# Kernel optimization log

Hardware: AMD Instinct MI355X
Metric: run time of the kernel (lower is better)

Reference implementation:

```python
import jax, jax.numpy as jnp
import numpy as np

# ---- static config (mirrors init_kwargs) ----
H, N, HKV = 32, 64, 8
HN = H * N            # model dim 2048
KV_DIM = HKV * N      # 512
B, T = 2, 1024
EPS = 1e-6
ROPE_THETA = 1.0e6
SPLITS_WAVGK = (96, 96, 64, 256, 64)   # xw, xa, xv, xg, xk lora ranks
SPLITS_RKV = (HN, KV_DIM, KV_DIM)


def rms_norm(x, w, eps=EPS):
    xf = x.astype(jnp.float32)
    var = jnp.mean(xf * xf, axis=-1, keepdims=True)
    return (w * (xf * jax.lax.rsqrt(var + eps))).astype(x.dtype)


def rotate_half(x):
    x1, x2 = jnp.split(x, 2, axis=-1)
    return jnp.concatenate((-x2, x1), axis=-1)


def apply_rope(q, k, cos, sin):
    # q:[B,T,H,N], k:[B,T,HKV,N], cos/sin:[B,T,N] -> unsqueeze head dim (unsqueeze_dim=2)
    cos = cos[:, :, None, :]
    sin = sin[:, :, None, :]
    return q * cos + rotate_half(q) * sin, k * cos + rotate_half(k) * sin


def rwkv7_recurrence(r, gk, k, v, a, b, S0):
    # fused_recurrent_rwkv7 (head_first=False). All inputs [B,T,H,N] fp32, S0 [B,H,N_key,N_val].
    # S_t = diag(exp(gk_t)) S_{t-1} + b_t (a_t^T S_{t-1}) + k_t v_t^T ;  o_t = r_t^T S_t
    def step(S, inp):
        r_t, w_t, k_t, v_t, a_t, b_t = inp
        sa = jnp.einsum('bhk,bhkv->bhv', a_t, S)
        S = (jnp.exp(w_t)[..., None] * S
             + k_t[..., None] * v_t[..., None, :]
             + b_t[..., None] * sa[..., None, :])
        o = jnp.einsum('bhk,bhkv->bhv', r_t, S)
        return S, o
    xs = tuple(jnp.swapaxes(t, 0, 1) for t in (r, gk, k, v, a, b))  # [T,B,H,N]
    S, o = jax.lax.scan(step, S0, xs)
    return jnp.swapaxes(o, 0, 1), S


def setup_inputs() -> dict:
    key = jax.random.key(0)
    ks = jax.random.split(key, 24)
    f32 = jnp.float32
    rn = lambda k, shape, s=1.0: jax.random.normal(k, shape, dtype=f32) * s

    x_in = rn(ks[0], (B, T, HN))
    v_first = rn(ks[1], (B, T, HKV, N))
    k_first = rn(ks[2], (B, T, HKV, N))
    state = jnp.zeros((B, H, N, N), f32)

    # real rope cache (faithful to get_batch_rope_cache output) at positions 0..T-1
    inv_freq = 1.0 / (ROPE_THETA ** (np.arange(0, N, 2, dtype=np.float32) / N))
    freqs = np.outer(np.arange(T, dtype=np.float32), inv_freq)  # [T, N/2]
    emb = np.concatenate([freqs, freqs], axis=-1)               # [T, N]
    calc_cos = jnp.broadcast_to(jnp.asarray(np.cos(emb), dtype=np.float32), (B, T, N))
    calc_sin = jnp.broadcast_to(jnp.asarray(np.sin(emb), dtype=np.float32), (B, T, N))

    wavgk1 = rn(ks[3], (HN, sum(SPLITS_WAVGK)), 0.02)
    w0 = rn(ks[4], (HN,), 0.5)
    w2 = rn(ks[5], (SPLITS_WAVGK[0], HN), 0.02)
    a0 = rn(ks[6], (HN,), 0.1)
    a2 = rn(ks[7], (SPLITS_WAVGK[1], HN), 0.02)
    v0 = rn(ks[8], (KV_DIM,), 0.1)
    v2 = rn(ks[9], (SPLITS_WAVGK[2], KV_DIM), 0.02)
    g2 = rn(ks[10], (SPLITS_WAVGK[3], HN), 0.02)
    k0 = rn(ks[11], (KV_DIM,), 0.1)
    k2 = rn(ks[12], (SPLITS_WAVGK[4], KV_DIM), 0.02)
    r_k = rn(ks[13], (H, N), 0.1)
    RKV = rn(ks[14], (HN, HN + 2 * KV_DIM), 0.02)   # fpx weight, dequantized form
    O = rn(ks[15], (HN, HN), 0.02)
    R_bias = rn(ks[16], (HN,), 0.02)
    K_bias = rn(ks[17], (KV_DIM,), 0.02)
    V_bias = rn(ks[18], (KV_DIM,), 0.02)
    ln_r = jnp.ones((N,), f32)
    ln_k = jnp.ones((N,), f32)
    ln1 = jnp.ones((HN,), f32)
    ln2 = jnp.ones((HN,), f32)

    return dict(x_in=x_in, v_first=v_first, k_first=k_first, state=state,
                calc_cos=calc_cos, calc_sin=calc_sin, wavgk1=wavgk1,
                w0=w0, w2=w2, a0=a0, a2=a2, v0=v0, v2=v2, g2=g2, k0=k0, k2=k2,
                r_k=r_k, RKV=RKV, O=O, R_bias=R_bias, K_bias=K_bias, V_bias=V_bias,
                ln_r=ln_r, ln_k=ln_k, ln1=ln1, ln2=ln2)


def reference(x_in, v_first, k_first, state, calc_cos, calc_sin, wavgk1,
              w0, w2, a0, a2, v0, v2, g2, k0, k2, r_k, RKV, O,
              R_bias, K_bias, V_bias, ln_r, ln_k, ln1, ln2):
    Bx, Tx, C = x_in.shape
    kv_repeat = HN // KV_DIM  # GQA repeat factor (4)

    x = rms_norm(x_in, ln1)
    xw, xa, xv, xg, xk = jnp.split(x @ wavgk1, np.cumsum(SPLITS_WAVGK)[:-1].tolist(), axis=-1)

    rkv = x @ RKV  # fpx_matmul -> dense matmul on dequantized weight
    r, k, v = jnp.split(rkv, np.cumsum(SPLITS_RKV)[:-1].tolist(), axis=-1)
    r = (r + R_bias).reshape(Bx, Tx, H, N)
    k = (k + K_bias).reshape(Bx, Tx, HKV, N)
    v = (v + V_bias).reshape(Bx, Tx, HKV, N)

    r = rms_norm(r, ln_r)
    k = rms_norm(k, ln_k)
    r, k = apply_rope(r, k, calc_cos, calc_sin)

    # layer_id = 1 (> 0): mix with first-layer value/key
    v = v + (v_first - v) * jax.nn.sigmoid(xv @ v2 + v0).reshape(Bx, Tx, HKV, N)
    k = k + (k_first - k) * jax.nn.sigmoid(xk @ k2 + k0).reshape(Bx, Tx, HKV, N)

    # repeat_kv: [B,T,HKV,N] -> [B,T,H,N] -> [B,T,HN]
    k = jnp.repeat(k, kv_repeat, axis=2).reshape(Bx, Tx, HN)
    v = jnp.repeat(v, kv_repeat, axis=2).reshape(Bx, Tx, HN)

    a = jax.nn.sigmoid(xa @ a2 + a0)  # in-context learning rate gate [B,T,HN]
    k4 = k.reshape(Bx, Tx, H, N)
    kk = (k4 / jnp.maximum(jnp.linalg.norm(k4, axis=-1, keepdims=True), 1e-12)).reshape(Bx, Tx, HN)

    w_log = -jax.nn.softplus(-(jnp.tanh(xw) @ w2 + w0)) - 0.5  # log-decay, <= -0.5
    k = k * (1.0 - w_log + a)
    aa = -kk
    bb = kk * a
    gk = -jnp.exp(w_log.astype(jnp.float32))  # passed to fused_recurrent_rwkv7 as log decay

    shp = (Bx, Tx, H, N)
    o, state_out = rwkv7_recurrence(
        r.reshape(shp).astype(jnp.float32), gk.reshape(shp),
        k.reshape(shp).astype(jnp.float32), v.reshape(shp).astype(jnp.float32),
        aa.reshape(shp).astype(jnp.float32), bb.reshape(shp).astype(jnp.float32),
        state.astype(jnp.float32))

    xx = o.reshape(Bx, Tx, HN) * (float(N) ** -0.5)
    bonus = ((r * k.reshape(shp) * r_k).sum(axis=-1, keepdims=True) * v.reshape(shp)).reshape(Bx, Tx, HN)
    xx = xx.astype(x_in.dtype) + bonus

    out = (xx * (jax.nn.sigmoid(xg) @ g2)) @ O  # fpx output projection
    x_new = x_in + out
    return rms_norm(x_new, ln2)
```

## Files before the change

### kernel.cpp

```cpp
#include <hip/hip_runtime.h>

typedef unsigned short u16;
typedef unsigned int u32;

using f32x4 = __attribute__((ext_vector_type(4))) float;
using bf16x8 = __attribute__((ext_vector_type(8))) __bf16;

#define HN 2048
#define KVD 512
#define TOKENS 2048
#define N1 3712
#define K2W 576
#define N2 7168

#define OFF_Y1   0ull
#define OFF_OO   0ull
#define OFF_XG   16777216ull
#define OFF_Y2   30408704ull
#define OFF_OUTR 30408704ull
#define OFF_BT1  89128960ull
#define OFF_XB   104333312ull
#define OFF_W2T  89128960ull
#define OFF_X2   97386496ull
#define OFF_OT   89128960ull
#define OFF_RR   112721920ull
#define OFF_DEC  129499136ull
#define OFF_KR   146276352ull
#define OFF_VV   163053568ull
#define OFF_AA   179830784ull
#define OFF_BB   196608000ull
#define WS_NEED  213385216ull

__device__ __forceinline__ u16 f2bf(float f) {
    u32 u = __float_as_uint(f);
    u32 r = u + 0x7fffu + ((u >> 16) & 1u);
    return (u16)(r >> 16);
}
__device__ __forceinline__ float sigm(float x) { return 1.f / (1.f + expf(-x)); }
__device__ __forceinline__ float wsum(float v) {
#pragma unroll
    for (int m = 32; m > 0; m >>= 1) v += __shfl_xor(v, m, 64);
    return v;
}
__device__ __forceinline__ float rowsum16(float v) {
    float t;
    t = __uint_as_float(__builtin_amdgcn_update_dpp(0, __float_as_uint(v), 0x121, 0xf, 0xf, true));
    v += t;
    t = __uint_as_float(__builtin_amdgcn_update_dpp(0, __float_as_uint(v), 0x122, 0xf, 0xf, true));
    v += t;
    t = __uint_as_float(__builtin_amdgcn_update_dpp(0, __float_as_uint(v), 0x124, 0xf, 0xf, true));
    v += t;
    t = __uint_as_float(__builtin_amdgcn_update_dpp(0, __float_as_uint(v), 0x128, 0xf, 0xf, true));
    v += t;
    return v;
}

typedef __attribute__((address_space(1))) const void glob_t;
typedef __attribute__((address_space(3))) void lds_t;
__device__ __forceinline__ void gload_lds16(const void* g, void* l) {
    __builtin_amdgcn_global_load_lds((glob_t*)g, (lds_t*)l, 16, 0, 0);
}

template<int OFF>
__device__ __forceinline__ float4 ds_read128(u32 a) {
    float4 r;
    asm volatile("ds_read_b128 %0, %1 offset:%2" : "=v"(r) : "v"(a), "i"(OFF));
    return r;
}
template<int OFF>
__device__ __forceinline__ float ds_read32(u32 a) {
    float r;
    asm volatile("ds_read_b32 %0, %1 offset:%2" : "=v"(r) : "v"(a), "i"(OFF));
    return r;
}

__global__ __launch_bounds__(256) void k_prep_bt1(const float* __restrict__ wavgk1,
                                                  const float* __restrict__ RKV,
                                                  u16* __restrict__ BT1) {
    __shared__ float tile[64][65];
    const int bn = blockIdx.x >> 5;
    const int bk = blockIdx.x & 31;
    const int n0 = bn << 6, k0 = bk << 6;
    const int c = threadIdx.x & 63, q = threadIdx.x >> 6;
#pragma unroll
    for (int i = 0; i < 16; ++i) {
        const int r = (q << 4) + i;
        float v = 0.f;
        if (bn < 9)       v = wavgk1[(size_t)(k0 + r) * 576 + n0 + c];
        else if (bn < 57) v = RKV[(size_t)(k0 + r) * 3072 + (n0 + c - 576)];
        tile[r][c] = v;
    }
    __syncthreads();
#pragma unroll
    for (int i = 0; i < 16; ++i) {
        const int rw = (q << 4) + i;
        BT1[(size_t)(n0 + rw) * 2048 + k0 + c] = f2bf(tile[c][rw]);
    }
}

__global__ __launch_bounds__(256) void k_prep_w2t(const float* __restrict__ w2, const float* __restrict__ a2,
                                                  const float* __restrict__ g2, const float* __restrict__ v2,
                                                  const float* __restrict__ k2, u16* __restrict__ W2T) {
    int idx = blockIdx.x * 256 + threadIdx.x;
    int n = idx / 576, c = idx - n * 576;
    float v = 0.f;
    if (n < 2048)      { if (c < 96)              v = w2[(size_t)c * 2048 + n]; }
    else if (n < 4096) { if (c >= 96 && c < 192)  v = a2[(size_t)(c - 96) * 2048 + (n - 2048)]; }
    else if (n < 6144) { if (c >= 192 && c < 448) v = g2[(size_t)(c - 192) * 2048 + (n - 4096)]; }
    else if (n < 6656) { if (c >= 448 && c < 512) v = v2[(size_t)(c - 448) * 512 + (n - 6144)]; }
    else               { if (c >= 512)            v = k2[(size_t)(c - 512) * 512 + (n - 6656)]; }
    W2T[idx] = f2bf(v);
}

__global__ __launch_bounds__(256) void k_prep_ot(const float* __restrict__ O, u16* __restrict__ OT) {
    __shared__ float tile[64][65];
    const int bn = blockIdx.x >> 5, bk = blockIdx.x & 31;
    const int n0 = bn << 6, k0 = bk << 6;
    const int c = threadIdx.x & 63, q = threadIdx.x >> 6;
#pragma unroll
    for (int i = 0; i < 16; ++i) {
        const int r = (q << 4) + i;
        tile[r][c] = O[(size_t)(k0 + r) * 2048 + n0 + c];
    }
    __syncthreads();
#pragma unroll
    for (int i = 0; i < 16; ++i) {
        const int rw = (q << 4) + i;
        OT[(size_t)(n0 + rw) * 2048 + k0 + c] = f2bf(tile[c][rw]);
    }
}

__global__ __launch_bounds__(256) void k_rms1(const float* __restrict__ X,
                                              const float* __restrict__ ln1,
                                              u16* __restrict__ XB) {
    const int t = blockIdx.x, tid = threadIdx.x;
    const float* row = X + ((size_t)t << 11);
    float4 v0 = *(const float4*)(row + tid * 8);
    float4 v1 = *(const float4*)(row + tid * 8 + 4);
    float ss = v0.x*v0.x + v0.y*v0.y + v0.z*v0.z + v0.w*v0.w
             + v1.x*v1.x + v1.y*v1.y + v1.z*v1.z + v1.w*v1.w;
    ss = wsum(ss);
    __shared__ float red[4];
    if ((tid & 63) == 0) red[tid >> 6] = ss;
    __syncthreads();
    float scale = rsqrtf((red[0] + red[1] + red[2] + red[3]) * (1.f / 2048.f) + 1e-6f);
    float4 w0_ = *(const float4*)(ln1 + tid * 8);
    float4 w1_ = *(const float4*)(ln1 + tid * 8 + 4);
    u16* o = XB + ((size_t)t << 11) + tid * 8;
    o[0] = f2bf(v0.x * scale * w0_.x); o[1] = f2bf(v0.y * scale * w0_.y);
    o[2] = f2bf(v0.z * scale * w0_.z); o[3] = f2bf(v0.w * scale * w0_.w);
    o[4] = f2bf(v1.x * scale * w1_.x); o[5] = f2bf(v1.y * scale * w1_.y);
    o[6] = f2bf(v1.z * scale * w1_.z); o[7] = f2bf(v1.w * scale * w1_.w);
}

__global__ __launch_bounds__(256) void k_gemm(const u16* __restrict__ A,
                                              const u16* __restrict__ Bt,
                                              float* __restrict__ C,
                                              int M, int N, int K) {
    __shared__ __align__(16) u16 tA[4096];
    __shared__ __align__(16) u16 tB[4096];
    const int tid = threadIdx.x;
    const int w = tid >> 6, l = tid & 63;
    const int bm = blockIdx.x << 7, bn = blockIdx.y << 7;
    const int wm = (w >> 1) << 6, wn = (w & 1) << 6;
    const int lrow = l >> 2;
    const int lk = (((l & 3) ^ ((l >> 3) & 3)) << 3);
    f32x4 acc[4][4] = {};
    const size_t rA0 = (size_t)(bm + (w << 4) + lrow) * K;
    const size_t rA1 = (size_t)(bm + ((w + 4) << 4) + lrow) * K;
    const size_t rB0 = (size_t)(bn + (w << 4) + lrow) * K;
    const size_t rB1 = (size_t)(bn + ((w + 4) << 4) + lrow) * K;
    const int frow = l & 15;
    const int koff = (((l >> 4) ^ ((l >> 1) & 3)) << 3);
    for (int kt = 0; kt < K; kt += 32) {
        gload_lds16(A + rA0 + kt + lk, &tA[w << 9]);
        gload_lds16(A + rA1 + kt + lk, &tA[2048 + (w << 9)]);
        gload_lds16(Bt + rB0 + kt + lk, &tB[w << 9]);
        gload_lds16(Bt + rB1 + kt + lk, &tB[2048 + (w << 9)]);
        __syncthreads();
        bf16x8 av[4], bv[4];
#pragma unroll
        for (int i = 0; i < 4; ++i) {
            av[i] = *(const bf16x8*)&tA[((wm + (i << 4) + frow) << 5) + koff];
            bv[i] = *(const bf16x8*)&tB[((wn + (i << 4) + frow) << 5) + koff];
        }
#pragma unroll
        for (int i = 0; i < 4; ++i)
#pragma unroll
            for (int j = 0; j < 4; ++j)
                acc[i][j] = __builtin_amdgcn_mfma_f32_16x16x32_bf16(av[i], bv[j], acc[i][j], 0, 0, 0);
        __syncthreads();
    }
    const int crow = bm + wm + ((l >> 4) << 2);
    const int ccol = bn + wn + (l & 15);
#pragma unroll
    for (int i = 0; i < 4; ++i)
#pragma unroll
        for (int j = 0; j < 4; ++j)
#pragma unroll
            for (int jj = 0; jj < 4; ++jj)
                C[(size_t)(crow + (i << 4) + jj) * N + ccol + (j << 4)] = acc[i][j][jj];
}

__global__ __launch_bounds__(256) void k_gemm2(const u16* __restrict__ A,
                                               const u16* __restrict__ Bt,
                                               float* __restrict__ C) {
    __shared__ __align__(16) u16 tA[4096];
    __shared__ __align__(16) u16 tB[4096];
    const int tid = threadIdx.x;
    const int w = tid >> 6, l = tid & 63;
    const int by = blockIdx.y;
    int c0, K;
    if (by < 16)      { c0 = 0;   K = 96; }
    else if (by < 32) { c0 = 96;  K = 96; }
    else if (by < 48) { c0 = 192; K = 256; }
    else if (by < 52) { c0 = 448; K = 64; }
    else              { c0 = 512; K = 64; }
    const int n0 = by << 7;
    const int bm = blockIdx.x << 7;
    const int wm = (w >> 1) << 6, wn = (w & 1) << 6;
    const int lrow = l >> 2;
    const int lk = (((l & 3) ^ ((l >> 3) & 3)) << 3);
    f32x4 acc[4][4] = {};
    const size_t rA0 = (size_t)(bm + (w << 4) + lrow) * 576 + c0;
    const size_t rA1 = (size_t)(bm + ((w + 4) << 4) + lrow) * 576 + c0;
    const size_t rB0 = (size_t)(n0 + (w << 4) + lrow) * 576 + c0;
    const size_t rB1 = (size_t)(n0 + ((w + 4) << 4) + lrow) * 576 + c0;
    const int frow = l & 15;
    const int koff = (((l >> 4) ^ ((l >> 1) & 3)) << 3);
    for (int kt = 0; kt < K; kt += 32) {
        gload_lds16(A + rA0 + kt + lk, &tA[w << 9]);
        gload_lds16(A + rA1 + kt + lk, &tA[2048 + (w << 9)]);
        gload_lds16(Bt + rB0 + kt + lk, &tB[w << 9]);
        gload_lds16(Bt + rB1 + kt + lk, &tB[2048 + (w << 9)]);
        __syncthreads();
        bf16x8 av[4], bv[4];
#pragma unroll
        for (int i = 0; i < 4; ++i) {
            av[i] = *(const bf16x8*)&tA[((wm + (i << 4) + frow) << 5) + koff];
            bv[i] = *(const bf16x8*)&tB[((wn + (i << 4) + frow) << 5) + koff];
        }
#pragma unroll
        for (int i = 0; i < 4; ++i)
#pragma unroll
            for (int j = 0; j < 4; ++j)
                acc[i][j] = __builtin_amdgcn_mfma_f32_16x16x32_bf16(av[i], bv[j], acc[i][j], 0, 0, 0);
        __syncthreads();
    }
    const int crow = bm + wm + ((l >> 4) << 2);
    const int ccol = n0 + wn + (l & 15);
#pragma unroll
    for (int i = 0; i < 4; ++i)
#pragma unroll
        for (int j = 0; j < 4; ++j)
#pragma unroll
            for (int jj = 0; jj < 4; ++jj)
                C[(size_t)(crow + (i << 4) + jj) * N2 + ccol + (j << 4)] = acc[i][j][jj];
}

__global__ __launch_bounds__(256) void k_prep_x2(const float* __restrict__ Y1, u16* __restrict__ X2) {
    int idx = blockIdx.x * 256 + threadIdx.x;
    int t = idx / 576, c = idx - t * 576;
    const float* y1 = Y1 + (size_t)t * N1;
    float v;
    if (c < 96)       v = tanhf(y1[c]);
    else if (c < 192) v = y1[c];
    else if (c < 448) v = sigm(y1[c + 64]);
    else if (c < 512) v = y1[c - 256];
    else              v = y1[c];
    X2[idx] = f2bf(v);
}

__global__ __launch_bounds__(256) void k_prep_rec(
    const float* __restrict__ Y1, const float* __restrict__ Y2,
    const float* __restrict__ v_first, const float* __restrict__ k_first,
    const float* __restrict__ cosb, const float* __restrict__ sinb,
    const float* __restrict__ w0, const float* __restrict__ a0,
    const float* __restrict__ v0b, const float* __restrict__ k0b,
    const float* __restrict__ R_bias, const float* __restrict__ K_bias,
    const float* __restrict__ V_bias, const float* __restrict__ ln_r,
    const float* __restrict__ ln_k,
    float* __restrict__ RR, float* __restrict__ DEC, float* __restrict__ KR,
    float* __restrict__ VV, float* __restrict__ AA, float* __restrict__ BB) {
    const int t = blockIdx.x, tid = threadIdx.x;
    const int ww = tid >> 6, lane = tid & 63;
    const float* y1 = Y1 + (size_t)t * N1;
    const float* y2 = Y2 + (size_t)t * N2;
    const float cs = cosb[t * 64 + lane];
    const float sn = sinb[t * 64 + lane];
    const float sign = lane < 32 ? -1.f : 1.f;
    const size_t tb = (size_t)t << 11;
    __shared__ float kkv[512], vkv[512];
#pragma unroll
    for (int i = 0; i < 8; ++i) {
        int h = ww * 8 + i, c = h * 64 + lane;
        float rr = y1[576 + c] + R_bias[c];
        float ssq = wsum(rr * rr);
        float rn = ln_r[lane] * rr * rsqrtf(ssq * (1.f / 64.f) + 1e-6f);
        float rot = sign * __shfl(rn, lane ^ 32, 64);
        RR[tb + c] = rn * cs + rot * sn;
    }
#pragma unroll
    for (int i = 0; i < 2; ++i) {
        int j = ww * 2 + i, c = j * 64 + lane;
        float kr = y1[2624 + c] + K_bias[c];
        float ssq = wsum(kr * kr);
        float kn = ln_k[lane] * kr * rsqrtf(ssq * (1.f / 64.f) + 1e-6f);
        float rot = sign * __shfl(kn, lane ^ 32, 64);
        float krope = kn * cs + rot * sn;
        float ksig = sigm(y2[6656 + c] + k0b[c]);
        kkv[c] = krope + (k_first[(size_t)t * 512 + c] - krope) * ksig;
        float vr = y1[3136 + c] + V_bias[c];
        float vsig = sigm(y2[6144 + c] + v0b[c]);
        vkv[c] = vr + (v_first[(size_t)t * 512 + c] - vr) * vsig;
    }
    __syncthreads();
#pragma unroll
    for (int i = 0; i < 8; ++i) {
        int h = ww * 8 + i, c = h * 64 + lane;
        int ckv = (h >> 2) * 64 + lane;
        float kb = kkv[ckv], vb = vkv[ckv];
        float a_ = sigm(y2[2048 + c] + a0[c]);
        float wr = y2[c] + w0[c];
        float z = -wr;
        float sp = fmaxf(z, 0.f) + log1pf(expf(-fabsf(z)));
        float w_log = -sp - 0.5f;
        float ssq = wsum(kb * kb);
        float kk = kb / fmaxf(sqrtf(ssq), 1e-12f);
        DEC[tb + c] = expf(-expf(w_log));
        KR[tb + c] = kb * (1.f - w_log + a_);
        VV[tb + c] = vb;
        AA[tb + c] = -kk;
        BB[tb + c] = kk * a_;
    }
}

__global__ __launch_bounds__(256, 1) void k_recv12(
    const float* __restrict__ RRp, const float* __restrict__ DECp,
    const float* __restrict__ KRp, const float* __restrict__ VVp,
    const float* __restrict__ AAp, const float* __restrict__ BBp,
    const float* __restrict__ S0, float* __restrict__ OO) {
    __shared__ __align__(16) float cbuf[2][6][32][64];
    const int tid = threadIdx.x;
    const int wl = tid >> 6;
    const int lane = tid & 63;
    const int vl = lane >> 4;
    const int kq = lane & 15;
    const int quarter = blockIdx.x & 3;
    const int ch = blockIdx.x >> 2;
    const int vcol = (quarter << 4) + (wl << 2) + vl;
    const size_t cb = ((size_t)(ch >> 5) * 1024 * 2048) + ((size_t)(ch & 31) << 6);

    const float* s0 = S0 + ((size_t)ch << 12);
    float L0 = s0[((kq << 2) + 0) * 64 + vcol];
    float L1 = s0[((kq << 2) + 1) * 64 + vcol];
    float L2 = s0[((kq << 2) + 2) * 64 + vcol];
    float L3 = s0[((kq << 2) + 3) * 64 + vcol];

    const float* gsrc[6] = {AAp, DECp, KRp, BBp, RRp, VVp};
    const int trow = (wl << 2) + vl;

#define STG(B, T0)                                                             \
    {                                                                          \
        const size_t g0 = cb + (size_t)((T0) + trow) * 2048 + (kq << 2);       \
        const size_t g1 = cb + (size_t)((T0) + 16 + trow) * 2048 + (kq << 2);  \
        float* lb = &cbuf[B][0][0][0] + (wl << 8);                             \
        _Pragma("unroll") for (int ar = 0; ar < 6; ++ar) {                     \
            gload_lds16(gsrc[ar] + g0, lb + ar * 2048);                        \
            gload_lds16(gsrc[ar] + g1, lb + ar * 2048 + 1024);                 \
        }                                                                      \
    }

    const u32 base0 = (u32)(size_t)(void*)&cbuf[0][0][0][0];
    const u32 aA0 = base0 + (kq << 4);
    const u32 aV0 = base0 + 40960 + (vcol << 2);

#define LDSTEP(J)                                                              \
    cA[J] = ds_read128<(J) * 256>(aA);                                         \
    cD[J] = ds_read128<8192 + (J) * 256>(aA);                                  \
    cK[J] = ds_read128<16384 + (J) * 256>(aA);                                 \
    cB[J] = ds_read128<24576 + (J) * 256>(aA);                                 \
    cR[J] = ds_read128<32768 + (J) * 256>(aA);                                 \
    cV[J] = ds_read32<(J) * 256>(aV);

    STG(0, 0);
    __syncthreads();

    for (int c = 0; c < 32; ++c) {
        const int b = c & 1;
        if (c < 31) STG(b ^ 1, (c + 1) << 5);
        u32 aA = aA0 + b * 49152;
        u32 aV = aV0 + b * 49152;
        int t = c << 5;
        for (int g = 0; g < 4; ++g) {
            float4 cA[8], cD[8], cK[8], cB[8], cR[8];
            float cV[8];
            LDSTEP(0) LDSTEP(1) LDSTEP(2) LDSTEP(3)
            LDSTEP(4) LDSTEP(5) LDSTEP(6) LDSTEP(7)
            asm volatile("s_waitcnt lgkmcnt(0)" ::: "memory");
            __builtin_amdgcn_sched_barrier(0);
#pragma unroll
            for (int j = 0; j < 8; ++j) {
                const float4 A4 = cA[j], D4 = cD[j], K4 = cK[j], B4 = cB[j], R4 = cR[j];
                const float Vsj = cV[j];
                float sp = fmaf(L1, A4.y, L0 * A4.x) + fmaf(L3, A4.w, L2 * A4.z);
                const float sa = rowsum16(sp);
                L0 = fmaf(B4.x, sa, fmaf(K4.x, Vsj, L0 * D4.x));
                L1 = fmaf(B4.y, sa, fmaf(K4.y, Vsj, L1 * D4.y));
                L2 = fmaf(B4.z, sa, fmaf(K4.z, Vsj, L2 * D4.z));
                L3 = fmaf(B4.w, sa, fmaf(K4.w, Vsj, L3 * D4.w));
                float op = fmaf(L1, R4.y, L0 * R4.x) + fmaf(L3, R4.w, L2 * R4.z);
                const float o = rowsum16(op);
                if (kq == 0) OO[cb + ((size_t)(t + j) << 11) + vcol] = o;
            }
            t += 8;
            aA += 2048;
            aV += 2048;
        }
        __syncthreads();
    }
#undef LDSTEP
#undef STG
}

__global__ __launch_bounds__(256) void k_gate(
    const float* __restrict__ OOp, const float* __restrict__ RRp,
    const float* __restrict__ KRp, const float* __restrict__ VVp,
    const float* __restrict__ Y2, const float* __restrict__ r_k,
    u16* __restrict__ XG) {
    const int t = blockIdx.x, tid = threadIdx.x;
    const int ww = tid >> 6, lane = tid & 63;
    const size_t tb = (size_t)t << 11;
#pragma unroll
    for (int i = 0; i < 8; ++i) {
        int c = (ww * 8 + i) * 64 + lane;
        float pr = RRp[tb + c] * KRp[tb + c] * r_k[c];
        float dot = wsum(pr);
        float xx = OOp[tb + c] * 0.125f + dot * VVp[tb + c];
        float g = Y2[(size_t)t * N2 + 4096 + c];
        XG[tb + c] = f2bf(xx * g);
    }
}

__global__ __launch_bounds__(256) void k_final(const float* __restrict__ x_in,
                                               const float* __restrict__ OUTR,
                                               const float* __restrict__ ln2,
                                               float* __restrict__ out) {
    const int t = blockIdx.x, tid = threadIdx.x;
    const float* xr = x_in + ((size_t)t << 11);
    const float* orow = OUTR + ((size_t)t << 11);
    float4 a0 = *(const float4*)(xr + tid * 8);
    float4 a1 = *(const float4*)(xr + tid * 8 + 4);
    float4 b0 = *(const float4*)(orow + tid * 8);
    float4 b1 = *(const float4*)(orow + tid * 8 + 4);
    float v[8] = {a0.x + b0.x, a0.y + b0.y, a0.z + b0.z, a0.w + b0.w,
                  a1.x + b1.x, a1.y + b1.y, a1.z + b1.z, a1.w + b1.w};
    float ss = 0.f;
#pragma unroll
    for (int i = 0; i < 8; ++i) ss = fmaf(v[i], v[i], ss);
    ss = wsum(ss);
    __shared__ float red[4];
    if ((tid & 63) == 0) red[tid >> 6] = ss;
    __syncthreads();
    float scale = rsqrtf((red[0] + red[1] + red[2] + red[3]) * (1.f / 2048.f) + 1e-6f);
    float* o = out + ((size_t)t << 11) + tid * 8;
#pragma unroll
    for (int i = 0; i < 8; ++i) o[i] = ln2[tid * 8 + i] * v[i] * scale;
}

extern "C" void kernel_launch(void* const* d_in, const int* in_sizes, int n_in,
                              void* d_out, int out_size, void* d_ws, size_t ws_size,
                              hipStream_t stream) {
    const float* x_in    = (const float*)d_in[0];
    const float* v_first = (const float*)d_in[1];
    const float* k_first = (const float*)d_in[2];
    const float* state   = (const float*)d_in[3];
    const float* cosb    = (const float*)d_in[4];
    const float* sinb    = (const float*)d_in[5];
    const float* wavgk1  = (const float*)d_in[6];
    const float* w0      = (const float*)d_in[7];
    const float* w2      = (const float*)d_in[8];
    const float* a0      = (const float*)d_in[9];
    const float* a2      = (const float*)d_in[10];
    const float* v0      = (const float*)d_in[11];
    const float* v2      = (const float*)d_in[12];
    const float* g2      = (const float*)d_in[13];
    const float* k0      = (const float*)d_in[14];
    const float* k2      = (const float*)d_in[15];
    const float* r_k     = (const float*)d_in[16];
    const float* RKV     = (const float*)d_in[17];
    const float* O       = (const float*)d_in[18];
    const float* R_bias  = (const float*)d_in[19];
    const float* K_bias  = (const float*)d_in[20];
    const float* V_bias  = (const float*)d_in[21];
    const float* ln_r    = (const float*)d_in[22];
    const float* ln_k    = (const float*)d_in[23];
    const float* ln1     = (const float*)d_in[24];
    const float* ln2     = (const float*)d_in[25];

    if (ws_size < WS_NEED) return;

    char* ws = (char*)d_ws;
    u16*   BT1  = (u16*)(ws + OFF_BT1);
    u16*   W2T  = (u16*)(ws + OFF_W2T);
    u16*   OT   = (u16*)(ws + OFF_OT);
    u16*   XB   = (u16*)(ws + OFF_XB);
    float* Y1   = (float*)(ws + OFF_Y1);
    u16*   X2   = (u16*)(ws + OFF_X2);
    float* Y2   = (float*)(ws + OFF_Y2);
    float* RR   = (float*)(ws + OFF_RR);
    float* DEC  = (float*)(ws + OFF_DEC);
    float* KR   = (float*)(ws + OFF_KR);
    float* VV   = (float*)(ws + OFF_VV);
    float* AA   = (float*)(ws + OFF_AA);
    float* BB   = (float*)(ws + OFF_BB);
    float* OO   = (float*)(ws + OFF_OO);
    u16*   XG   = (u16*)(ws + OFF_XG);
    float* OUTR = (float*)(ws + OFF_OUTR);

    k_prep_bt1<<<1856, 256, 0, stream>>>(wavgk1, RKV, BT1);
    k_rms1<<<2048, 256, 0, stream>>>(x_in, ln1, XB);
    k_gemm<<<dim3(16, 29), 256, 0, stream>>>(XB, BT1, Y1, 2048, N1, 2048);
    k_prep_w2t<<<16128, 256, 0, stream>>>(w2, a2, g2, v2, k2, W2T);
    k_prep_x2<<<4608, 256, 0, stream>>>(Y1, X2);
    k_gemm2<<<dim3(16, 56), 256, 0, stream>>>(X2, W2T, Y2);
    k_prep_rec<<<2048, 256, 0, stream>>>(Y1, Y2, v_first, k_first, cosb, sinb,
                                         w0, a0, v0, k0, R_bias, K_bias, V_bias,
                                         ln_r, ln_k, RR, DEC, KR, VV, AA, BB);
    k_prep_ot<<<1024, 256, 0, stream>>>(O, OT);
    k_recv12<<<256, 256, 0, stream>>>(RR, DEC, KR, VV, AA, BB, state, OO);
    k_gate<<<2048, 256, 0, stream>>>(OO, RR, KR, VV, Y2, r_k, XG);
    k_gemm<<<dim3(16, 16), 256, 0, stream>>>(XG, OT, OUTR, 2048, 2048, 2048);
    k_final<<<2048, 256, 0, stream>>>(x_in, OUTR, ln2, (float*)d_out);
}
```

Measured before the change: 384.8 us.

## Process two value columns per thread in RWKV7 recurrence, halving block size

The recurrence kernel now gives each thread two adjacent value columns of the state instead of one, so each block runs 128 threads instead of 256. Every LDS read of the per-step a/decay/k/b/r vectors is reused for two columns, and the chunk staging is split across two waves, each loading three arrays. The aim is to cut LDS read traffic and wave count per state slice. In exchange each thread carries more serial work per step, twice the rowsum shuffle chains and more registers, which could lengthen the dependent recurrence path with fewer waves to hide latency.

```diff
diff --git a/kernel.cpp b/kernel.cpp
--- a/kernel.cpp
+++ b/kernel.cpp
@@ -68,9 +68,9 @@
     return r;
 }
 template<int OFF>
-__device__ __forceinline__ float ds_read32(u32 a) {
-    float r;
-    asm volatile("ds_read_b32 %0, %1 offset:%2" : "=v"(r) : "v"(a), "i"(OFF));
+__device__ __forceinline__ float2 ds_read64(u32 a) {
+    float2 r;
+    asm volatile("ds_read_b64 %0, %1 offset:%2" : "=v"(r) : "v"(a), "i"(OFF));
     return r;
 }
 
@@ -335,7 +335,7 @@
     }
 }
 
-__global__ __launch_bounds__(256, 1) void k_recv12(
+__global__ __launch_bounds__(128, 1) void k_recv13(
     const float* __restrict__ RRp, const float* __restrict__ DECp,
     const float* __restrict__ KRp, const float* __restrict__ VVp,
     const float* __restrict__ AAp, const float* __restrict__ BBp,
@@ -348,32 +348,34 @@
     const int kq = lane & 15;
     const int quarter = blockIdx.x & 3;
     const int ch = blockIdx.x >> 2;
-    const int vcol = (quarter << 4) + (wl << 2) + vl;
+    const int vcol2 = (quarter << 4) + (wl << 3) + (vl << 1);
     const size_t cb = ((size_t)(ch >> 5) * 1024 * 2048) + ((size_t)(ch & 31) << 6);
 
     const float* s0 = S0 + ((size_t)ch << 12);
-    float L0 = s0[((kq << 2) + 0) * 64 + vcol];
-    float L1 = s0[((kq << 2) + 1) * 64 + vcol];
-    float L2 = s0[((kq << 2) + 2) * 64 + vcol];
-    float L3 = s0[((kq << 2) + 3) * 64 + vcol];
-
-    const float* gsrc[6] = {AAp, DECp, KRp, BBp, RRp, VVp};
-    const int trow = (wl << 2) + vl;
+    float2 L0 = *(const float2*)(s0 + ((kq << 2) + 0) * 64 + vcol2);
+    float2 L1 = *(const float2*)(s0 + ((kq << 2) + 1) * 64 + vcol2);
+    float2 L2 = *(const float2*)(s0 + ((kq << 2) + 2) * 64 + vcol2);
+    float2 L3 = *(const float2*)(s0 + ((kq << 2) + 3) * 64 + vcol2);
+
+    const float* sA = wl ? BBp : AAp;
+    const float* sB = wl ? RRp : DECp;
+    const float* sC = wl ? VVp : KRp;
 
 #define STG(B, T0)                                                             \
     {                                                                          \
-        const size_t g0 = cb + (size_t)((T0) + trow) * 2048 + (kq << 2);       \
-        const size_t g1 = cb + (size_t)((T0) + 16 + trow) * 2048 + (kq << 2);  \
-        float* lb = &cbuf[B][0][0][0] + (wl << 8);                             \
-        _Pragma("unroll") for (int ar = 0; ar < 6; ++ar) {                     \
-            gload_lds16(gsrc[ar] + g0, lb + ar * 2048);                        \
-            gload_lds16(gsrc[ar] + g1, lb + ar * 2048 + 1024);                 \
+        float* lb = &cbuf[B][0][0][0] + wl * 6144;                             \
+        _Pragma("unroll") for (int r0 = 0; r0 < 32; r0 += 4) {                 \
+            const size_t g = cb + (size_t)((T0) + r0 + (lane >> 4)) * 2048     \
+                           + ((lane & 15) << 2);                               \
+            gload_lds16(sA + g, lb + (r0 << 6));                               \
+            gload_lds16(sB + g, lb + 2048 + (r0 << 6));                        \
+            gload_lds16(sC + g, lb + 4096 + (r0 << 6));                        \
         }                                                                      \
     }
 
     const u32 base0 = (u32)(size_t)(void*)&cbuf[0][0][0][0];
     const u32 aA0 = base0 + (kq << 4);
-    const u32 aV0 = base0 + 40960 + (vcol << 2);
+    const u32 aV0 = base0 + 40960 + (vcol2 << 2);
 
 #define LDSTEP(J)                                                              \
     cA[J] = ds_read128<(J) * 256>(aA);                                         \
@@ -381,7 +383,7 @@
     cK[J] = ds_read128<16384 + (J) * 256>(aA);                                 \
     cB[J] = ds_read128<24576 + (J) * 256>(aA);                                 \
     cR[J] = ds_read128<32768 + (J) * 256>(aA);                                 \
-    cV[J] = ds_read32<(J) * 256>(aV);
+    cV[J] = ds_read64<(J) * 256>(aV);
 
     STG(0, 0);
     __syncthreads();
@@ -394,7 +396,7 @@
         int t = c << 5;
         for (int g = 0; g < 4; ++g) {
             float4 cA[8], cD[8], cK[8], cB[8], cR[8];
-            float cV[8];
+            float2 cV[8];
             LDSTEP(0) LDSTEP(1) LDSTEP(2) LDSTEP(3)
             LDSTEP(4) LDSTEP(5) LDSTEP(6) LDSTEP(7)
             asm volatile("s_waitcnt lgkmcnt(0)" ::: "memory");
@@ -402,16 +404,25 @@
 #pragma unroll
             for (int j = 0; j < 8; ++j) {
                 const float4 A4 = cA[j], D4 = cD[j], K4 = cK[j], B4 = cB[j], R4 = cR[j];
-                const float Vsj = cV[j];
-                float sp = fmaf(L1, A4.y, L0 * A4.x) + fmaf(L3, A4.w, L2 * A4.z);
-                const float sa = rowsum16(sp);
-                L0 = fmaf(B4.x, sa, fmaf(K4.x, Vsj, L0 * D4.x));
-                L1 = fmaf(B4.y, sa, fmaf(K4.y, Vsj, L1 * D4.y));
-                L2 = fmaf(B4.z, sa, fmaf(K4.z, Vsj, L2 * D4.z));
-                L3 = fmaf(B4.w, sa, fmaf(K4.w, Vsj, L3 * D4.w));
-                float op = fmaf(L1, R4.y, L0 * R4.x) + fmaf(L3, R4.w, L2 * R4.z);
-                const float o = rowsum16(op);
-                if (kq == 0) OO[cb + ((size_t)(t + j) << 11) + vcol] = o;
+                const float2 Vj = cV[j];
+                float spx = fmaf(L1.x, A4.y, L0.x * A4.x) + fmaf(L3.x, A4.w, L2.x * A4.z);
+                float spy = fmaf(L1.y, A4.y, L0.y * A4.x) + fmaf(L3.y, A4.w, L2.y * A4.z);
+                const float sax = rowsum16(spx);
+                const float say = rowsum16(spy);
+                L0.x = fmaf(B4.x, sax, fmaf(K4.x, Vj.x, L0.x * D4.x));
+                L0.y = fmaf(B4.x, say, fmaf(K4.x, Vj.y, L0.y * D4.x));
+                L1.x = fmaf(B4.y, sax, fmaf(K4.y, Vj.x, L1.x * D4.y));
+                L1.y = fmaf(B4.y, say, fmaf(K4.y, Vj.y, L1.y * D4.y));
+                L2.x = fmaf(B4.z, sax, fmaf(K4.z, Vj.x, L2.x * D4.z));
+                L2.y = fmaf(B4.z, say, fmaf(K4.z, Vj.y, L2.y * D4.z));
+                L3.x = fmaf(B4.w, sax, fmaf(K4.w, Vj.x, L3.x * D4.w));
+                L3.y = fmaf(B4.w, say, fmaf(K4.w, Vj.y, L3.y * D4.w));
+                float opx = fmaf(L1.x, R4.y, L0.x * R4.x) + fmaf(L3.x, R4.w, L2.x * R4.z);
+                float opy = fmaf(L1.y, R4.y, L0.y * R4.x) + fmaf(L3.y, R4.w, L2.y * R4.z);
+                const float ox = rowsum16(opx);
+                const float oy = rowsum16(opy);
+                if (kq == 0)
+                    *(float2*)&OO[cb + ((size_t)(t + j) << 11) + vcol2] = make_float2(ox, oy);
             }
             t += 8;
             aA += 2048;
@@ -528,7 +539,7 @@
                                          w0, a0, v0, k0, R_bias, K_bias, V_bias,
                                          ln_r, ln_k, RR, DEC, KR, VV, AA, BB);
     k_prep_ot<<<1024, 256, 0, stream>>>(O, OT);
-    k_recv12<<<256, 256, 0, stream>>>(RR, DEC, KR, VV, AA, BB, state, OO);
+    k_recv13<<<256, 128, 0, stream>>>(RR, DEC, KR, VV, AA, BB, state, OO);
     k_gate<<<2048, 256, 0, stream>>>(OO, RR, KR, VV, Y2, r_k, XG);
     k_gemm<<<dim3(16, 16), 256, 0, stream>>>(XG, OT, OUTR, 2048, 2048, 2048);
     k_final<<<2048, 256, 0, stream>>>(x_in, OUTR, ln2, (float*)d_out);
```

Result: slower. 416.8 us (+8.3%).
